# Optimization experiments

Measured on AMD Instinct MI355X. Metric: run time of the kernel, lower is better.

The kernel has to match this reference:

```python
import jax, jax.numpy as jnp
import numpy as np

N = 50000
E = 600000
F_IN = 128
HID = 128
N_CLS = 16


def setup_inputs() -> dict:
    key = jax.random.key(0)
    ks = jax.random.split(key, 12)
    x = jax.random.normal(ks[0], (N, F_IN), dtype=jnp.float32)
    edge_index = jax.random.randint(ks[1], (2, E), 0, N, dtype=jnp.int64)
    def glorot(k, shape):
        lim = float(np.sqrt(6.0 / (shape[0] + shape[1])))
        return jax.random.uniform(k, shape, jnp.float32, -lim, lim)
    return {
        "x": x,
        "edge_index": edge_index,
        "W1": glorot(ks[2], (F_IN, HID)), "b1": jnp.zeros((HID,), jnp.float32),
        "W2": glorot(ks[3], (HID, HID)), "b2": jnp.zeros((HID,), jnp.float32),
        "W3": glorot(ks[4], (HID, HID)), "b3": jnp.zeros((HID,), jnp.float32),
        "Wlin": glorot(ks[5], (HID, N_CLS)), "blin": jnp.zeros((N_CLS,), jnp.float32),
    }


def _gcn_norm(edge_index, n_nodes):
    # PyG GCNConv default: add self-loops, symmetric normalization
    loops = jnp.arange(n_nodes, dtype=edge_index.dtype)
    src = jnp.concatenate([edge_index[0], loops])  # [E+N]
    dst = jnp.concatenate([edge_index[1], loops])  # [E+N]
    deg = jax.ops.segment_sum(jnp.ones_like(dst, dtype=jnp.float32), dst,
                              num_segments=n_nodes)
    dis = jnp.where(deg > 0, jax.lax.rsqrt(jnp.maximum(deg, 1.0)), 0.0)
    norm = dis[src] * dis[dst]  # [E+N]
    return src, dst, norm


def _gcn_conv(h, src, dst, norm, n_nodes, W, b):
    h = h @ W                                   # transform first (small GEMM)
    msg = h[src] * norm[:, None]                # gather + scale, [E+N, HID]
    out = jax.ops.segment_sum(msg, dst, num_segments=n_nodes)  # scatter-add
    return out + b


def reference(x, edge_index, W1, b1, W2, b2, W3, b3, Wlin, blin):
    n_nodes = x.shape[0]
    src, dst, norm = _gcn_norm(edge_index, n_nodes)
    h = jax.nn.relu(_gcn_conv(x, src, dst, norm, n_nodes, W1, b1))
    h = jax.nn.relu(_gcn_conv(h, src, dst, norm, n_nodes, W2, b2))
    h = _gcn_conv(h, src, dst, norm, n_nodes, W3, b3)
    return h @ Wlin + blin  # [N, N_CLS]
```

## Files before the change

kernel.cpp:

```cpp
#include <hip/hip_runtime.h>
#include <hip/hip_fp16.h>


#define FD 128
#define NCLS 16

__global__ __launch_bounds__(256) void k_init_deg(int* __restrict__ degi, int n) {
  int i = blockIdx.x * 256 + threadIdx.x;
  if (i < n) degi[i] = 1;
}

__global__ __launch_bounds__(256) void k_count(const int* __restrict__ dst,
                                               int* __restrict__ degi, int e) {
  int i = blockIdx.x * 256 + threadIdx.x;
  if (i < e) atomicAdd(&degi[dst[i]], 1);
}

__global__ __launch_bounds__(256) void k_dis(const int* __restrict__ degi,
                                             float* __restrict__ dis, int n) {
  int i = blockIdx.x * 256 + threadIdx.x;
  if (i < n) dis[i] = rsqrtf((float)degi[i]);
}

__global__ __launch_bounds__(1024) void k_scanA(const int* __restrict__ degi,
                                                int* __restrict__ ptr,
                                                int* __restrict__ bsum, int n) {
  __shared__ int buf[1024];
  int tid = threadIdx.x;
  int i = blockIdx.x * 1024 + tid;
  int v = (i < n) ? (degi[i] - 1) : 0;
  buf[tid] = v;
  __syncthreads();
  for (int off = 1; off < 1024; off <<= 1) {
    int t = (tid >= off) ? buf[tid - off] : 0;
    __syncthreads();
    buf[tid] += t;
    __syncthreads();
  }
  if (i < n) ptr[i] = buf[tid] - v;
  if (tid == 1023) bsum[blockIdx.x] = buf[1023];
}

__global__ void k_scanB(int* __restrict__ bsum, int nb) {
  if (threadIdx.x == 0 && blockIdx.x == 0) {
    int run = 0;
    for (int b = 0; b < nb; ++b) { int t = bsum[b]; bsum[b] = run; run += t; }
  }
}

__global__ __launch_bounds__(256) void k_scanC(int* __restrict__ ptr,
                                               int* __restrict__ cur,
                                               const int* __restrict__ bsum,
                                               int n, int e) {
  int i = blockIdx.x * 256 + threadIdx.x;
  if (i < n) {
    int p = ptr[i] + bsum[i >> 10];
    ptr[i] = p;
    cur[i] = p;
  }
  if (i == 0) ptr[n] = e;
}

__global__ __launch_bounds__(256) void k_fill(const int* __restrict__ src,
                                              const int* __restrict__ dst,
                                              int* __restrict__ cur,
                                              const float* __restrict__ dis,
                                              int2* __restrict__ sn, int e) {
  int i = blockIdx.x * 256 + threadIdx.x;
  if (i < e) {
    int s = src[i], d = dst[i];
    int p = atomicAdd(&cur[d], 1);
    sn[p] = make_int2(s, __float_as_int(dis[s] * dis[d]));
  }
}

__global__ __launch_bounds__(256) void k_gemm128h(const float* __restrict__ in,
                                                  const float* __restrict__ W,
                                                  __half* __restrict__ outh, int n) {
  __shared__ float4 wl[FD][16];
  int tid = threadIdx.x;
  int cbase = blockIdx.y * 64;
  int cb4 = cbase >> 2;
  const float4* W4 = reinterpret_cast<const float4*>(W);
  for (int i = tid; i < FD * 16; i += 256) {
    int k = i >> 4, cg = i & 15;
    wl[k][cg] = W4[k * 32 + cb4 + cg];
  }
  __syncthreads();

  int cg = tid & 15;
  int rg = tid >> 4;
  int rbase = blockIdx.x * 64 + rg * 4;
  const float* rowp[4];
#pragma unroll
  for (int r = 0; r < 4; ++r) {
    int row = rbase + r;
    if (row > n - 1) row = n - 1;
    rowp[r] = in + (size_t)row * FD;
  }
  float4 acc[4];
#pragma unroll
  for (int r = 0; r < 4; ++r) acc[r] = make_float4(0.f, 0.f, 0.f, 0.f);

  float4 a_cur[4];
#pragma unroll
  for (int r = 0; r < 4; ++r) a_cur[r] = *reinterpret_cast<const float4*>(rowp[r]);

  for (int k = 0; k < FD; k += 4) {
    int kn = (k + 4 < FD) ? k + 4 : k;
    float4 a_nxt[4];
#pragma unroll
    for (int r = 0; r < 4; ++r)
      a_nxt[r] = *reinterpret_cast<const float4*>(rowp[r] + kn);
    float4 w0 = wl[k + 0][cg];
    float4 w1 = wl[k + 1][cg];
    float4 w2 = wl[k + 2][cg];
    float4 w3 = wl[k + 3][cg];
#pragma unroll
    for (int r = 0; r < 4; ++r) {
      float4 a = a_cur[r];
      acc[r].x = fmaf(a.x, w0.x, acc[r].x);
      acc[r].y = fmaf(a.x, w0.y, acc[r].y);
      acc[r].z = fmaf(a.x, w0.z, acc[r].z);
      acc[r].w = fmaf(a.x, w0.w, acc[r].w);
      acc[r].x = fmaf(a.y, w1.x, acc[r].x);
      acc[r].y = fmaf(a.y, w1.y, acc[r].y);
      acc[r].z = fmaf(a.y, w1.z, acc[r].z);
      acc[r].w = fmaf(a.y, w1.w, acc[r].w);
      acc[r].x = fmaf(a.z, w2.x, acc[r].x);
      acc[r].y = fmaf(a.z, w2.y, acc[r].y);
      acc[r].z = fmaf(a.z, w2.z, acc[r].z);
      acc[r].w = fmaf(a.z, w2.w, acc[r].w);
      acc[r].x = fmaf(a.w, w3.x, acc[r].x);
      acc[r].y = fmaf(a.w, w3.y, acc[r].y);
      acc[r].z = fmaf(a.w, w3.z, acc[r].z);
      acc[r].w = fmaf(a.w, w3.w, acc[r].w);
      a_cur[r] = a_nxt[r];
    }
  }

#pragma unroll
  for (int r = 0; r < 4; ++r) {
    int row = rbase + r;
    if (row < n) {
      __half h[4];
      h[0] = __float2half_rn(acc[r].x);
      h[1] = __float2half_rn(acc[r].y);
      h[2] = __float2half_rn(acc[r].z);
      h[3] = __float2half_rn(acc[r].w);
      *reinterpret_cast<uint2*>(&outh[(size_t)row * FD + cbase + cg * 4]) =
          *reinterpret_cast<uint2*>(h);
    }
  }
}

__device__ __forceinline__ void agg_wave(const __half* __restrict__ t,
                                         const int* __restrict__ ptr,
                                         const int2* __restrict__ sn,
                                         int node, int lane, float o[4]) {
  int h = lane >> 5;
  int q = lane & 31;
  float a0 = 0.f, a1 = 0.f, a2 = 0.f, a3 = 0.f;
  int e0 = ptr[node], e1 = ptr[node + 1];
  for (int base = e0; base < e1; base += 16) {
    int s[8];
    float w[8];
#pragma unroll
    for (int j = 0; j < 8; ++j) {
      int idx = base + 2 * j + h;
      if (idx < e1) {
        int2 p = sn[idx];
        s[j] = p.x;
        w[j] = __int_as_float(p.y);
      } else {
        s[j] = node;
        w[j] = 0.f;
      }
    }
    ushort4 v[8];
#pragma unroll
    for (int j = 0; j < 8; ++j)
      v[j] = *reinterpret_cast<const ushort4*>(&t[(size_t)s[j] * FD + q * 4]);
#pragma unroll
    for (int j = 0; j < 8; ++j) {
      a0 = fmaf(__half2float(__ushort_as_half(v[j].x)), w[j], a0);
      a1 = fmaf(__half2float(__ushort_as_half(v[j].y)), w[j], a1);
      a2 = fmaf(__half2float(__ushort_as_half(v[j].z)), w[j], a2);
      a3 = fmaf(__half2float(__ushort_as_half(v[j].w)), w[j], a3);
    }
  }
  o[0] = a0 + __shfl(a0, lane ^ 32, 64);
  o[1] = a1 + __shfl(a1, lane ^ 32, 64);
  o[2] = a2 + __shfl(a2, lane ^ 32, 64);
  o[3] = a3 + __shfl(a3, lane ^ 32, 64);
}

__global__ __launch_bounds__(256) void k_agg(const __half* __restrict__ t,
                                             const int* __restrict__ ptr,
                                             const int2* __restrict__ sn,
                                             const float* __restrict__ dis,
                                             const float* __restrict__ bias,
                                             float* __restrict__ out, int relu) {
  int lane = threadIdx.x & 63;
  int node = blockIdx.x * 4 + (threadIdx.x >> 6);
  float d = dis[node];
  float dd = d * d;
  float o[4];
  agg_wave(t, ptr, sn, node, lane, o);
  if (lane < 32) {
    int q = lane;
    ushort4 sv = *reinterpret_cast<const ushort4*>(&t[(size_t)node * FD + q * 4]);
    float4 b = *reinterpret_cast<const float4*>(&bias[q * 4]);
    o[0] = fmaf(__half2float(__ushort_as_half(sv.x)), dd, o[0]) + b.x;
    o[1] = fmaf(__half2float(__ushort_as_half(sv.y)), dd, o[1]) + b.y;
    o[2] = fmaf(__half2float(__ushort_as_half(sv.z)), dd, o[2]) + b.z;
    o[3] = fmaf(__half2float(__ushort_as_half(sv.w)), dd, o[3]) + b.w;
    if (relu) {
      o[0] = fmaxf(o[0], 0.f);
      o[1] = fmaxf(o[1], 0.f);
      o[2] = fmaxf(o[2], 0.f);
      o[3] = fmaxf(o[3], 0.f);
    }
    float4 r = make_float4(o[0], o[1], o[2], o[3]);
    *reinterpret_cast<float4*>(&out[(size_t)node * FD + q * 4]) = r;
  }
}

__global__ __launch_bounds__(256) void k_agg_lin(const __half* __restrict__ t,
                                                 const int* __restrict__ ptr,
                                                 const int2* __restrict__ sn,
                                                 const float* __restrict__ dis,
                                                 const float* __restrict__ b3,
                                                 const float* __restrict__ Wl,
                                                 const float* __restrict__ bl,
                                                 float* __restrict__ out) {
  __shared__ float hl[4][FD];
  int wid = threadIdx.x >> 6;
  int lane = threadIdx.x & 63;
  int node = blockIdx.x * 4 + wid;
  float d = dis[node];
  float dd = d * d;
  float o[4];
  agg_wave(t, ptr, sn, node, lane, o);
  if (lane < 32) {
    int q = lane;
    ushort4 sv = *reinterpret_cast<const ushort4*>(&t[(size_t)node * FD + q * 4]);
    float4 b = *reinterpret_cast<const float4*>(&b3[q * 4]);
    hl[wid][q * 4 + 0] = fmaf(__half2float(__ushort_as_half(sv.x)), dd, o[0]) + b.x;
    hl[wid][q * 4 + 1] = fmaf(__half2float(__ushort_as_half(sv.y)), dd, o[1]) + b.y;
    hl[wid][q * 4 + 2] = fmaf(__half2float(__ushort_as_half(sv.z)), dd, o[2]) + b.z;
    hl[wid][q * 4 + 3] = fmaf(__half2float(__ushort_as_half(sv.w)), dd, o[3]) + b.w;
  }
  __syncthreads();
  int c = lane & 15, kc = lane >> 4;
  float s = 0.f;
#pragma unroll
  for (int k0 = 0; k0 < 32; ++k0) {
    int k = kc * 32 + k0;
    s = fmaf(hl[wid][k], Wl[k * NCLS + c], s);
  }
  s += __shfl(s, lane ^ 16, 64);
  s += __shfl(s, lane ^ 32, 64);
  if (lane < NCLS)
    out[(size_t)node * NCLS + lane] = s + bl[lane];
}

extern "C" void kernel_launch(void* const* d_in, const int* in_sizes, int n_in,
                              void* d_out, int out_size, void* d_ws, size_t ws_size,
                              hipStream_t stream) {
  const float* x  = (const float*)d_in[0];
  const int*   ei = (const int*)d_in[1];
  const float* W1 = (const float*)d_in[2];
  const float* b1 = (const float*)d_in[3];
  const float* W2 = (const float*)d_in[4];
  const float* b2 = (const float*)d_in[5];
  const float* W3 = (const float*)d_in[6];
  const float* b3 = (const float*)d_in[7];
  const float* Wl = (const float*)d_in[8];
  const float* bl = (const float*)d_in[9];
  float* out = (float*)d_out;

  const int n = in_sizes[0] / FD;
  const int e = in_sizes[1] / 2;
  const int* src = ei;
  const int* dst = ei + e;

  __half* th  = (__half*)d_ws;
  float* bufH = (float*)(th + (size_t)n * FD);
  int*   degi = (int*)(bufH + (size_t)n * FD);
  float* dis  = (float*)(degi + n);
  int*   ptr  = (int*)(dis + n);
  int*   cur  = ptr + n + 1;
  int*   bsum = cur + n;
  int2*  sn   = (int2*)(((uintptr_t)(bsum + 64) + 15) & ~(uintptr_t)15);

  const int gn = (n + 255) / 256;
  const int ge = (e + 255) / 256;
  const int nb = (n + 1023) / 1024;

  k_init_deg<<<gn, 256, 0, stream>>>(degi, n);
  k_count<<<ge, 256, 0, stream>>>(dst, degi, e);
  k_dis<<<gn, 256, 0, stream>>>(degi, dis, n);
  k_scanA<<<nb, 1024, 0, stream>>>(degi, ptr, bsum, n);
  k_scanB<<<1, 64, 0, stream>>>(bsum, nb);
  k_scanC<<<gn, 256, 0, stream>>>(ptr, cur, bsum, n, e);
  k_fill<<<ge, 256, 0, stream>>>(src, dst, cur, dis, sn, e);

  dim3 gG((n + 63) / 64, 2);
  const int ga = n / 4;

  k_gemm128h<<<gG, 256, 0, stream>>>(x, W1, th, n);
  k_agg<<<ga, 256, 0, stream>>>(th, ptr, sn, dis, b1, bufH, 1);
  k_gemm128h<<<gG, 256, 0, stream>>>(bufH, W2, th, n);
  k_agg<<<ga, 256, 0, stream>>>(th, ptr, sn, dis, b2, bufH, 1);
  k_gemm128h<<<gG, 256, 0, stream>>>(bufH, W3, th, n);
  k_agg_lin<<<ga, 256, 0, stream>>>(th, ptr, sn, dis, b3, Wl, bl, out);
}
```

Measured before the change: 374.2 us.

## Use MFMA fp16 GEMM with fp16 activations and prepacked weights

Replaces the scalar FMA float GEMM with an MFMA 16x16x32 fp16 kernel that stages A rows in XOR-swizzled LDS and reads weights prepacked into the MFMA operand layout. Input x is converted to fp16 and the aggregation outputs are stored as fp16, halving the hidden-activation traffic between layers. This adds conversion kernels and lowers the precision of the GEMM inputs. Output stores become scattered 2-byte writes per lane.

```diff
diff --git a/kernel.cpp b/kernel.cpp
--- a/kernel.cpp
+++ b/kernel.cpp
@@ -4,6 +4,9 @@
 
 #define FD 128
 #define NCLS 16
+
+typedef _Float16 f16x8 __attribute__((ext_vector_type(8)));
+typedef float f32x4 __attribute__((ext_vector_type(4)));
 
 __global__ __launch_bounds__(256) void k_init_deg(int* __restrict__ degi, int n) {
   int i = blockIdx.x * 256 + threadIdx.x;
@@ -74,82 +77,80 @@
   }
 }
 
-__global__ __launch_bounds__(256) void k_gemm128h(const float* __restrict__ in,
-                                                  const float* __restrict__ W,
-                                                  __half* __restrict__ outh, int n) {
-  __shared__ float4 wl[FD][16];
+__global__ __launch_bounds__(256) void k_convx(const float* __restrict__ x,
+                                               __half* __restrict__ xh) {
+  int i = blockIdx.x * 256 + threadIdx.x;
+  int base = i * 8;
+  float4 a = *reinterpret_cast<const float4*>(&x[base]);
+  float4 b = *reinterpret_cast<const float4*>(&x[base + 4]);
+  __half h[8];
+  h[0] = __float2half_rn(a.x); h[1] = __float2half_rn(a.y);
+  h[2] = __float2half_rn(a.z); h[3] = __float2half_rn(a.w);
+  h[4] = __float2half_rn(b.x); h[5] = __float2half_rn(b.y);
+  h[6] = __float2half_rn(b.z); h[7] = __float2half_rn(b.w);
+  *reinterpret_cast<uint4*>(&xh[base]) = *reinterpret_cast<uint4*>(h);
+}
+
+__global__ __launch_bounds__(256) void k_convW(const float* __restrict__ W,
+                                               __half* __restrict__ wp) {
+  int i = blockIdx.x * 256 + threadIdx.x;
+  int j = i & 7;
+  int l = (i >> 3) & 63;
+  int kc = (i >> 9) & 3;
+  int c = i >> 11;
+  int k = kc * 32 + ((l >> 4) << 3) + j;
+  int col = c * 16 + (l & 15);
+  wp[i] = __float2half_rn(W[k * FD + col]);
+}
+
+__global__ __launch_bounds__(256) void k_gemm_mfma(const __half* __restrict__ A,
+                                                   const __half* __restrict__ Wp,
+                                                   __half* __restrict__ C, int n) {
+  __shared__ uint4 al4[1024];
+  __shared__ uint4 wl4[2048];
   int tid = threadIdx.x;
-  int cbase = blockIdx.y * 64;
-  int cb4 = cbase >> 2;
-  const float4* W4 = reinterpret_cast<const float4*>(W);
-  for (int i = tid; i < FD * 16; i += 256) {
-    int k = i >> 4, cg = i & 15;
-    wl[k][cg] = W4[k * 32 + cb4 + cg];
+  const uint4* wsrc = reinterpret_cast<const uint4*>(Wp);
+  for (int i = tid; i < 2048; i += 256) wl4[i] = wsrc[i];
+
+  int rbase_blk = blockIdx.x * 64;
+  for (int i = tid; i < 1024; i += 256) {
+    int row = i >> 4;
+    int b = (i & 15) << 4;
+    int grow = rbase_blk + row;
+    if (grow > n - 1) grow = n - 1;
+    uint4 v = *reinterpret_cast<const uint4*>(
+        reinterpret_cast<const char*>(A) + (size_t)grow * 256 + b);
+    *reinterpret_cast<uint4*>(
+        reinterpret_cast<char*>(al4) + row * 256 + (b ^ ((row & 7) << 4))) = v;
   }
   __syncthreads();
 
-  int cg = tid & 15;
-  int rg = tid >> 4;
-  int rbase = blockIdx.x * 64 + rg * 4;
-  const float* rowp[4];
-#pragma unroll
-  for (int r = 0; r < 4; ++r) {
-    int row = rbase + r;
-    if (row > n - 1) row = n - 1;
-    rowp[r] = in + (size_t)row * FD;
-  }
-  float4 acc[4];
-#pragma unroll
-  for (int r = 0; r < 4; ++r) acc[r] = make_float4(0.f, 0.f, 0.f, 0.f);
-
-  float4 a_cur[4];
-#pragma unroll
-  for (int r = 0; r < 4; ++r) a_cur[r] = *reinterpret_cast<const float4*>(rowp[r]);
-
-  for (int k = 0; k < FD; k += 4) {
-    int kn = (k + 4 < FD) ? k + 4 : k;
-    float4 a_nxt[4];
-#pragma unroll
-    for (int r = 0; r < 4; ++r)
-      a_nxt[r] = *reinterpret_cast<const float4*>(rowp[r] + kn);
-    float4 w0 = wl[k + 0][cg];
-    float4 w1 = wl[k + 1][cg];
-    float4 w2 = wl[k + 2][cg];
-    float4 w3 = wl[k + 3][cg];
+  int l = tid & 63, wid = tid >> 6;
+  int arow = wid * 16 + (l & 15);
+  f16x8 af[4];
+#pragma unroll
+  for (int kc = 0; kc < 4; ++kc) {
+    int b = kc * 64 + ((l >> 4) << 4);
+    af[kc] = *reinterpret_cast<const f16x8*>(
+        reinterpret_cast<const char*>(al4) + arow * 256 + (b ^ ((arow & 7) << 4)));
+  }
+
+  int rowout = rbase_blk + wid * 16 + ((l >> 4) << 2);
+  int colb = l & 15;
+  const __half* wl = reinterpret_cast<const __half*>(wl4);
+#pragma unroll
+  for (int c = 0; c < 8; ++c) {
+    f32x4 acc = {0.f, 0.f, 0.f, 0.f};
+#pragma unroll
+    for (int kc = 0; kc < 4; ++kc) {
+      f16x8 bf = *reinterpret_cast<const f16x8*>(&wl[((c * 4 + kc) * 64 + l) * 8]);
+      acc = __builtin_amdgcn_mfma_f32_16x16x32_f16(af[kc], bf, acc, 0, 0, 0);
+    }
+    int col = c * 16 + colb;
 #pragma unroll
     for (int r = 0; r < 4; ++r) {
-      float4 a = a_cur[r];
-      acc[r].x = fmaf(a.x, w0.x, acc[r].x);
-      acc[r].y = fmaf(a.x, w0.y, acc[r].y);
-      acc[r].z = fmaf(a.x, w0.z, acc[r].z);
-      acc[r].w = fmaf(a.x, w0.w, acc[r].w);
-      acc[r].x = fmaf(a.y, w1.x, acc[r].x);
-      acc[r].y = fmaf(a.y, w1.y, acc[r].y);
-      acc[r].z = fmaf(a.y, w1.z, acc[r].z);
-      acc[r].w = fmaf(a.y, w1.w, acc[r].w);
-      acc[r].x = fmaf(a.z, w2.x, acc[r].x);
-      acc[r].y = fmaf(a.z, w2.y, acc[r].y);
-      acc[r].z = fmaf(a.z, w2.z, acc[r].z);
-      acc[r].w = fmaf(a.z, w2.w, acc[r].w);
-      acc[r].x = fmaf(a.w, w3.x, acc[r].x);
-      acc[r].y = fmaf(a.w, w3.y, acc[r].y);
-      acc[r].z = fmaf(a.w, w3.z, acc[r].z);
-      acc[r].w = fmaf(a.w, w3.w, acc[r].w);
-      a_cur[r] = a_nxt[r];
-    }
-  }
-
-#pragma unroll
-  for (int r = 0; r < 4; ++r) {
-    int row = rbase + r;
-    if (row < n) {
-      __half h[4];
-      h[0] = __float2half_rn(acc[r].x);
-      h[1] = __float2half_rn(acc[r].y);
-      h[2] = __float2half_rn(acc[r].z);
-      h[3] = __float2half_rn(acc[r].w);
-      *reinterpret_cast<uint2*>(&outh[(size_t)row * FD + cbase + cg * 4]) =
-          *reinterpret_cast<uint2*>(h);
+      int row = rowout + r;
+      if (row < n) C[(size_t)row * FD + col] = __float2half_rn(acc[r]);
     }
   }
 }
@@ -200,7 +201,7 @@
                                              const int2* __restrict__ sn,
                                              const float* __restrict__ dis,
                                              const float* __restrict__ bias,
-                                             float* __restrict__ out, int relu) {
+                                             __half* __restrict__ out, int relu) {
   int lane = threadIdx.x & 63;
   int node = blockIdx.x * 4 + (threadIdx.x >> 6);
   float d = dis[node];
@@ -221,8 +222,13 @@
       o[2] = fmaxf(o[2], 0.f);
       o[3] = fmaxf(o[3], 0.f);
     }
-    float4 r = make_float4(o[0], o[1], o[2], o[3]);
-    *reinterpret_cast<float4*>(&out[(size_t)node * FD + q * 4]) = r;
+    __half hh[4];
+    hh[0] = __float2half_rn(o[0]);
+    hh[1] = __float2half_rn(o[1]);
+    hh[2] = __float2half_rn(o[2]);
+    hh[3] = __float2half_rn(o[3]);
+    *reinterpret_cast<uint2*>(&out[(size_t)node * FD + q * 4]) =
+        *reinterpret_cast<uint2*>(hh);
   }
 }
 
@@ -285,9 +291,13 @@
   const int* src = ei;
   const int* dst = ei + e;
 
-  __half* th  = (__half*)d_ws;
-  float* bufH = (float*)(th + (size_t)n * FD);
-  int*   degi = (int*)(bufH + (size_t)n * FD);
+  __half* thA = (__half*)d_ws;
+  __half* thB = thA + (size_t)n * FD;
+  __half* xh  = thB + (size_t)n * FD;
+  __half* wp1 = xh + (size_t)n * FD;
+  __half* wp2 = wp1 + 16384;
+  __half* wp3 = wp2 + 16384;
+  int*   degi = (int*)(wp3 + 16384);
   float* dis  = (float*)(degi + n);
   int*   ptr  = (int*)(dis + n);
   int*   cur  = ptr + n + 1;
@@ -306,13 +316,18 @@
   k_scanC<<<gn, 256, 0, stream>>>(ptr, cur, bsum, n, e);
   k_fill<<<ge, 256, 0, stream>>>(src, dst, cur, dis, sn, e);
 
-  dim3 gG((n + 63) / 64, 2);
+  k_convx<<<(n * FD) / 2048, 256, 0, stream>>>(x, xh);
+  k_convW<<<64, 256, 0, stream>>>(W1, wp1);
+  k_convW<<<64, 256, 0, stream>>>(W2, wp2);
+  k_convW<<<64, 256, 0, stream>>>(W3, wp3);
+
+  const int gG = (n + 63) / 64;
   const int ga = n / 4;
 
-  k_gemm128h<<<gG, 256, 0, stream>>>(x, W1, th, n);
-  k_agg<<<ga, 256, 0, stream>>>(th, ptr, sn, dis, b1, bufH, 1);
-  k_gemm128h<<<gG, 256, 0, stream>>>(bufH, W2, th, n);
-  k_agg<<<ga, 256, 0, stream>>>(th, ptr, sn, dis, b2, bufH, 1);
-  k_gemm128h<<<gG, 256, 0, stream>>>(bufH, W3, th, n);
-  k_agg_lin<<<ga, 256, 0, stream>>>(th, ptr, sn, dis, b3, Wl, bl, out);
-}
+  k_gemm_mfma<<<gG, 256, 0, stream>>>(xh, wp1, thA, n);
+  k_agg<<<ga, 256, 0, stream>>>(thA, ptr, sn, dis, b1, thB, 1);
+  k_gemm_mfma<<<gG, 256, 0, stream>>>(thB, wp2, thA, n);
+  k_agg<<<ga, 256, 0, stream>>>(thA, ptr, sn, dis, b2, thB, 1);
+  k_gemm_mfma<<<gG, 256, 0, stream>>>(thB, wp3, thA, n);
+  k_agg_lin<<<ga, 256, 0, stream>>>(thA, ptr, sn, dis, b3, Wl, bl, out);
+}
```

Result: faster. 325.6 us (-13.0%).
